# Kernel optimization log

Hardware: AMD Instinct MI355X
Metric: run time of the kernel (lower is better)

Reference implementation:

```python
import jax, jax.numpy as jnp
import numpy as np

N, E, D, H, L, FF = 50000, 500000, 128, 8, 2, 512
HD = D // H  # head dim = 16


def setup_inputs() -> dict:
    key = jax.random.key(0)
    ks = jax.random.split(key, 16)
    inp = {
        "x": jax.random.normal(ks[0], (N, D), jnp.float32),
        "edge_index": jax.random.randint(ks[1], (2, E), 0, N, jnp.int32),
    }
    def w(k, shape, fan_in):
        return jax.random.normal(k, shape, jnp.float32) / np.float32(np.sqrt(fan_in))
    inp["Wq"] = w(ks[2], (L, D, D), D)
    inp["Wk"] = w(ks[3], (L, D, D), D)
    inp["Wv"] = w(ks[4], (L, D, D), D)
    inp["Wo"] = w(ks[5], (L, D, D), D)
    inp["Wpos"] = w(ks[6], (L, D, D), D)
    inp["Wdeg"] = w(ks[7], (L, 1, D), 1)
    inp["W1"] = w(ks[8], (L, D, FF), D)
    inp["W2"] = w(ks[9], (L, FF, D), FF)
    for name, shape in [("bq", (L, D)), ("bk", (L, D)), ("bv", (L, D)),
                        ("bo", (L, D)), ("bpos", (L, D)), ("bdeg", (L, D)),
                        ("ln1_b", (L, D)), ("ln2_b", (L, D)),
                        ("b1", (L, FF)), ("b2", (L, D))]:
        inp[name] = jnp.zeros(shape, jnp.float32)
    inp["ln1_g"] = jnp.ones((L, D), jnp.float32)
    inp["ln2_g"] = jnp.ones((L, D), jnp.float32)
    return inp


def _layernorm(x, g, b):
    mu = jnp.mean(x, axis=-1, keepdims=True)
    var = jnp.mean(jnp.square(x - mu), axis=-1, keepdims=True)
    return (x - mu) * jax.lax.rsqrt(var + 1e-5) * g + b


def _forward(edge_index, x, Wq, bq, Wk, bk, Wv, bv, Wo, bo, Wpos, bpos,
             Wdeg, bdeg, ln1_g, ln1_b, ln2_g, ln2_b, W1, b1, W2, b2):
    n = x.shape[0]
    loops = jnp.arange(n, dtype=edge_index.dtype)
    src = jnp.concatenate([edge_index[0], loops])  # [E+N]
    dst = jnp.concatenate([edge_index[1], loops])  # [E+N]
    scale = np.float32(np.sqrt(HD))
    for l in range(L):
        # pre-attention LayerNorm
        xn = _layernorm(x, ln1_g[l], ln1_b[l])
        # positional encoding: x + proj(x) + deg_proj(standardized degree)
        deg = jax.ops.segment_sum(jnp.ones_like(src, dtype=x.dtype), src, num_segments=n)
        deg = (deg - deg.mean()) / (jnp.std(deg, ddof=1) + 1e-6)
        pos = xn @ Wpos[l] + bpos[l] + deg[:, None] * Wdeg[l][0] + bdeg[l]
        xp = xn + pos
        # per-node QKV projections (linear => identical to per-edge projection)
        q = (xp @ Wq[l] + bq[l]).reshape(n, H, HD)
        k = (xp @ Wk[l] + bk[l]).reshape(n, H, HD)
        v = (xp @ Wv[l] + bv[l]).reshape(n, H, HD)
        # per-edge attention logits  [E+N, H]
        att = jnp.einsum('ehd,ehd->eh', q[dst], k[src]) / scale
        att = jnp.nan_to_num(jnp.clip(att, -50.0, 50.0), nan=0.0, posinf=50.0, neginf=-50.0)
        # segment softmax over destination nodes (every node has a self loop)
        m = jax.ops.segment_max(att, dst, num_segments=n)        # [N, H]
        ex = jnp.exp(att - m[dst])
        s = jax.ops.segment_sum(ex, dst, num_segments=n)
        alpha = ex / (s[dst] + 1e-16)                             # [E+N, H]
        # weighted aggregation + output projection
        msg = (v[src] * alpha[:, :, None]).reshape(-1, D)         # [E+N, D]
        aggr = jax.ops.segment_sum(msg, dst, num_segments=n)      # [N, D]
        x = x + (aggr @ Wo[l] + bo[l])
        # FFN sublayer
        h = jax.nn.gelu(_layernorm(x, ln2_g[l], ln2_b[l]) @ W1[l] + b1[l], approximate=False)
        x = x + (h @ W2[l] + b2[l])
    return x


def reference(x, edge_index, Wq, bq, Wk, bk, Wv, bv, Wo, bo, Wpos, bpos,
              Wdeg, bdeg, ln1_g, ln1_b, ln2_g, ln2_b, W1, b1, W2, b2):
    return _forward(edge_index, x, Wq, bq, Wk, bk, Wv, bv, Wo, bo, Wpos, bpos,
                    Wdeg, bdeg, ln1_g, ln1_b, ln2_g, ln2_b, W1, b1, W2, b2)
```

## Files before the change

### kernel.cpp

```cpp
#include <hip/hip_runtime.h>
#include <hip/hip_bf16.h>
#include <hip/hip_fp16.h>
#include <math.h>

#define DMODEL 128
#define NHEAD 8
#define HEADD 16
#define NLAYER 2
#define FFDIM 512
#define MPAD 50048
#define QKVW 384

using short8 = __attribute__((ext_vector_type(8))) short;
using half8  = __attribute__((ext_vector_type(8))) _Float16;
using f32x4  = __attribute__((ext_vector_type(4))) float;

static __device__ __forceinline__ unsigned short f2h(float f) {
    __half h = __float2half(f);
    unsigned short u; __builtin_memcpy(&u, &h, 2); return u;
}
static __device__ __forceinline__ float h2f(unsigned short u) {
    __half h; __builtin_memcpy(&h, &u, 2); return __half2float(h);
}
static __device__ __forceinline__ half8 s2h8(short8 s) {
    half8 h; __builtin_memcpy(&h, &s, 16); return h;
}
static __device__ __forceinline__ f32x4 MFMAH(short8 a, short8 b, f32x4 c) {
    return __builtin_amdgcn_mfma_f32_16x16x32_f16(s2h8(a), s2h8(b), c, 0, 0, 0);
}
static __device__ __forceinline__ float gelu_fast(float v) {
    float u = v * (0.7978845608f + 0.0356774081f * v * v);
    float t = 1.0f - 2.0f / (1.0f + __expf(2.0f * u));
    return 0.5f * v * (1.0f + t);
}

__global__ __launch_bounds__(256)
void ln_kernel(const float* __restrict__ x, const float* __restrict__ g,
               const float* __restrict__ b, unsigned short* __restrict__ out, int n)
{
    int wave = threadIdx.x >> 6;
    int lane = threadIdx.x & 63;
    int row  = blockIdx.x * 4 + wave;
    if (row >= n) return;
    float2 xv = *(const float2*)(x + (size_t)row * DMODEL + lane * 2);
    float s  = xv.x + xv.y;
    float ss = xv.x * xv.x + xv.y * xv.y;
    #pragma unroll
    for (int d = 1; d < 64; d <<= 1) {
        s  += __shfl_xor(s, d);
        ss += __shfl_xor(ss, d);
    }
    float mu   = s * (1.0f / 128.0f);
    float var  = ss * (1.0f / 128.0f) - mu * mu;
    float rstd = rsqrtf(var + 1e-5f);
    float2 gv = *(const float2*)(g + lane * 2);
    float2 bv = *(const float2*)(b + lane * 2);
    ushort2 o;
    o.x = f2h((xv.x - mu) * rstd * gv.x + bv.x);
    o.y = f2h((xv.y - mu) * rstd * gv.y + bv.y);
    *(ushort2*)(out + (size_t)row * DMODEL + lane * 2) = o;
}

__global__ void wconv_all(const float* __restrict__ Wq, const float* __restrict__ Wk,
                          const float* __restrict__ Wv, const float* __restrict__ Wo,
                          const float* __restrict__ Wpos, const float* __restrict__ W1,
                          const float* __restrict__ W2,
                          unsigned short* __restrict__ wqkvt, unsigned short* __restrict__ wot,
                          unsigned short* __restrict__ wpt, unsigned short* __restrict__ w1t,
                          unsigned short* __restrict__ w2t)
{
    const int DD = NLAYER * DMODEL * DMODEL;
    const int DF = NLAYER * DMODEL * FFDIM;
    int i = blockIdx.x * 256 + threadIdx.x;
    if (i < 3 * DD) {
        int w = i / DD, r = i - w * DD;
        const float* src = (w == 0) ? Wq : (w == 1 ? Wk : Wv);
        int l = r >> 14, rr = r & 16383;
        int k = rr >> 7, nn = rr & 127;
        wqkvt[(size_t)l * QKVW * DMODEL + (size_t)(w * 128 + nn) * DMODEL + k] = f2h(src[r]);
    } else if (i < 5 * DD) {
        int w = (i - 3 * DD) / DD, r = (i - 3 * DD) - w * DD;
        const float* src = (w == 0) ? Wo : Wpos;
        unsigned short* dst = (w == 0) ? wot : wpt;
        int l = r >> 14, rr = r & 16383;
        int k = rr >> 7, nn = rr & 127;
        dst[(size_t)l * DMODEL * DMODEL + (size_t)nn * DMODEL + k] = f2h(src[r]);
    } else if (i < 5 * DD + DF) {
        int r = i - 5 * DD;
        int l = r >> 16, rr = r & 65535;
        int k = rr >> 9, nn = rr & 511;
        w1t[(size_t)l * FFDIM * DMODEL + (size_t)nn * DMODEL + k] = f2h(W1[r]);
    } else if (i < 5 * DD + 2 * DF) {
        int r = i - 5 * DD - DF;
        int l = r >> 16, rr = r & 65535;
        int k = rr >> 7, nn = rr & 127;
        w2t[(size_t)l * DMODEL * FFDIM + (size_t)nn * FFDIM + k] = f2h(W2[r]);
    }
}

__global__ void init_all(float* __restrict__ deg, int* __restrict__ counts,
                         float* __restrict__ stats, int n)
{
    int i = blockIdx.x * 256 + threadIdx.x;
    if (i < n) { deg[i] = 1.0f; counts[i] = 0; }
    if (i == 0) stats[0] = 0.f;
}

__global__ void edge_count(const int* __restrict__ ei, float* __restrict__ deg,
                           int* __restrict__ counts, int e, int n)
{
    int i = blockIdx.x * 256 + threadIdx.x;
    if (i < e) {
        atomicAdd(&deg[ei[i]], 1.0f);
        atomicAdd(&counts[ei[e + i]], 1);
    } else if (i < e + n) {
        atomicAdd(&counts[i - e], 1);
    }
}

__global__ __launch_bounds__(256)
void deg_var(const float* __restrict__ deg, float* __restrict__ stats, float mean, int n)
{
    float acc = 0.f;
    for (int i = blockIdx.x * blockDim.x + threadIdx.x; i < n; i += gridDim.x * blockDim.x) {
        float d = deg[i] - mean;
        acc += d * d;
    }
    #pragma unroll
    for (int d = 1; d < 64; d <<= 1) acc += __shfl_xor(acc, d);
    __shared__ float wsum[4];
    int lane = threadIdx.x & 63, wv = threadIdx.x >> 6;
    if (lane == 0) wsum[wv] = acc;
    __syncthreads();
    if (threadIdx.x == 0) atomicAdd(stats, wsum[0] + wsum[1] + wsum[2] + wsum[3]);
}

__global__ __launch_bounds__(256)
void scan_block(const int* __restrict__ in, int* __restrict__ out,
                int* __restrict__ sums, int n)
{
    __shared__ int buf[2][256];
    int t = threadIdx.x;
    int i = blockIdx.x * 256 + t;
    int v = (i < n) ? in[i] : 0;
    buf[0][t] = v;
    __syncthreads();
    int cur = 0;
    #pragma unroll
    for (int d = 1; d < 256; d <<= 1) {
        int val = buf[cur][t] + ((t >= d) ? buf[cur][t - d] : 0);
        buf[cur ^ 1][t] = val;
        cur ^= 1;
        __syncthreads();
    }
    if (i < n) out[i] = buf[cur][t] - v;
    if (t == 255 && sums) sums[blockIdx.x] = buf[cur][255];
}

__global__ void scan_add(int* __restrict__ offs, int* __restrict__ cursor,
                         const int* __restrict__ carry, int n)
{
    int i = blockIdx.x * 256 + threadIdx.x;
    if (i < n) {
        int v = offs[i] + carry[blockIdx.x];
        offs[i] = v;
        cursor[i] = v;
    }
}

__global__ void csr_fill(const int* __restrict__ ei, int* __restrict__ cursor,
                         int* __restrict__ csr_src, int e, int n)
{
    int i = blockIdx.x * 256 + threadIdx.x;
    if (i >= e + n) return;
    int d, s;
    if (i < e) { s = ei[i]; d = ei[e + i]; }
    else       { s = d = i - e; }
    int pos = atomicAdd(&cursor[d], 1);
    csr_src[pos] = s;
}

static __device__ __forceinline__ void ep_resln(
    f32x4 (&acc)[2][4], float* sm, int row0,
    int wr, int wc, int quad, int l15,
    const float* __restrict__ bias, const float* __restrict__ g,
    const float* __restrict__ bb,
    float* __restrict__ x, unsigned short* __restrict__ lnout, int n)
{
    #pragma unroll
    for (int i = 0; i < 2; ++i) {
        #pragma unroll
        for (int rr = 0; rr < 4; ++rr) {
            int rl = wr * 32 + i * 16 + quad * 4 + rr;
            size_t gr = (size_t)row0 + rl;
            float ps = 0.f, pq = 0.f;
            #pragma unroll
            for (int j = 0; j < 4; ++j) {
                int gc = wc * 64 + j * 16 + l15;
                float xv = (gr < (size_t)n) ? x[gr * DMODEL + gc] : 0.f;
                float v = acc[i][j][rr] + bias[gc] + xv;
                acc[i][j][rr] = v;
                ps += v; pq += v * v;
            }
            ps += __shfl_xor(ps, 1); pq += __shfl_xor(pq, 1);
            ps += __shfl_xor(ps, 2); pq += __shfl_xor(pq, 2);
            ps += __shfl_xor(ps, 4); pq += __shfl_xor(pq, 4);
            ps += __shfl_xor(ps, 8); pq += __shfl_xor(pq, 8);
            if (l15 == 0) { sm[(rl * 2 + wc) * 2 + 0] = ps; sm[(rl * 2 + wc) * 2 + 1] = pq; }
        }
    }
    __syncthreads();
    #pragma unroll
    for (int i = 0; i < 2; ++i) {
        #pragma unroll
        for (int rr = 0; rr < 4; ++rr) {
            int rl = wr * 32 + i * 16 + quad * 4 + rr;
            size_t gr = (size_t)row0 + rl;
            if (gr >= (size_t)n) continue;
            float su = sm[(rl * 2 + 0) * 2 + 0] + sm[(rl * 2 + 1) * 2 + 0];
            float sq = sm[(rl * 2 + 0) * 2 + 1] + sm[(rl * 2 + 1) * 2 + 1];
            float mu   = su * (1.f / 128.f);
            float var  = sq * (1.f / 128.f) - mu * mu;
            float rstd = rsqrtf(var + 1e-5f);
            #pragma unroll
            for (int j = 0; j < 4; ++j) {
                int gc = wc * 64 + j * 16 + l15;
                float v = acc[i][j][rr];
                x[gr * DMODEL + gc] = v;
                lnout[gr * DMODEL + gc] = f2h((v - mu) * rstd * g[gc] + bb[gc]);
            }
        }
    }
}

__global__ __launch_bounds__(256)
void pos_qkv(const unsigned short* __restrict__ xnb,
             const unsigned short* __restrict__ wpos,
             const unsigned short* __restrict__ wqkv,
             const float* __restrict__ bpos,
             const float* __restrict__ deg, const float* __restrict__ stats, float mean,
             const float* __restrict__ wdeg, const float* __restrict__ bdeg,
             const float* __restrict__ bq, const float* __restrict__ bk,
             const float* __restrict__ bv,
             unsigned short* __restrict__ qkv, int n)
{
    __shared__ __align__(16) unsigned short As[64 * 130];
    __shared__ __align__(16) unsigned short Bs[128 * 130];

    const int tid = threadIdx.x, wave = tid >> 6, lane = tid & 63;
    const int wr = wave >> 1, wc = wave & 1, quad = lane >> 4, l15 = lane & 15;
    const int row0 = blockIdx.x * 64;

    #pragma unroll
    for (int c = 0; c < 4; ++c) {
        int g = tid + c * 256; int r = g >> 4, col8 = g & 15;
        *(short8*)&As[r * 130 + col8 * 8] =
            *(const short8*)(xnb + (size_t)(row0 + r) * DMODEL + col8 * 8);
    }
    #pragma unroll
    for (int c = 0; c < 8; ++c) {
        int g = tid + c * 256; int r = g >> 4, col8 = g & 15;
        *(short8*)&Bs[r * 130 + col8 * 8] =
            *(const short8*)(wpos + (size_t)r * DMODEL + col8 * 8);
    }
    __syncthreads();

    short8 af[2][4], bfr[4][4];
    #pragma unroll
    for (int i = 0; i < 2; ++i)
        #pragma unroll
        for (int ks = 0; ks < 4; ++ks)
            af[i][ks] = *(const short8*)&As[(wr * 32 + i * 16 + l15) * 130 + (ks * 4 + quad) * 8];
    #pragma unroll
    for (int j = 0; j < 4; ++j)
        #pragma unroll
        for (int ks = 0; ks < 4; ++ks)
            bfr[j][ks] = *(const short8*)&Bs[(wc * 64 + j * 16 + l15) * 130 + (ks * 4 + quad) * 8];
    __syncthreads();

    f32x4 acc[2][4] = {};
    #pragma unroll
    for (int ks = 0; ks < 4; ++ks)
        #pragma unroll
        for (int i = 0; i < 2; ++i)
            #pragma unroll
            for (int j = 0; j < 4; ++j)
                acc[i][j] = MFMAH(af[i][ks], bfr[j][ks], acc[i][j]);

    {
        float sdv = sqrtf(stats[0] / (float)(n - 1)) + 1e-6f;
        #pragma unroll
        for (int i = 0; i < 2; ++i) {
            #pragma unroll
            for (int rr = 0; rr < 4; ++rr) {
                int rl = wr * 32 + i * 16 + quad * 4 + rr;
                size_t gr = (size_t)row0 + rl;
                if (gr >= (size_t)n) continue;
                float dg = (deg[gr] - mean) / sdv;
                #pragma unroll
                for (int j = 0; j < 4; ++j) {
                    int gc = wc * 64 + j * 16 + l15;
                    float xn = h2f(As[rl * 130 + gc]);
                    float val = acc[i][j][rr] + bpos[gc] + dg * wdeg[gc] + bdeg[gc] + xn;
                    As[rl * 130 + gc] = f2h(val);
                }
            }
        }
    }
    __syncthreads();

    short8 af2[2][4];
    #pragma unroll
    for (int i = 0; i < 2; ++i)
        #pragma unroll
        for (int ks = 0; ks < 4; ++ks)
            af2[i][ks] = *(const short8*)&As[(wr * 32 + i * 16 + l15) * 130 + (ks * 4 + quad) * 8];
    __syncthreads();

    #pragma unroll
    for (int c = 0; c < 3; ++c) {
        #pragma unroll
        for (int cc = 0; cc < 8; ++cc) {
            int g = tid + cc * 256; int r = g >> 4, col8 = g & 15;
            *(short8*)&Bs[r * 130 + col8 * 8] =
                *(const short8*)(wqkv + (size_t)(c * 128 + r) * DMODEL + col8 * 8);
        }
        __syncthreads();
        short8 bf2[4][4];
        #pragma unroll
        for (int j = 0; j < 4; ++j)
            #pragma unroll
            for (int ks = 0; ks < 4; ++ks)
                bf2[j][ks] = *(const short8*)&Bs[(wc * 64 + j * 16 + l15) * 130 + (ks * 4 + quad) * 8];

        f32x4 a2[2][4] = {};
        #pragma unroll
        for (int ks = 0; ks < 4; ++ks)
            #pragma unroll
            for (int i = 0; i < 2; ++i)
                #pragma unroll
                for (int j = 0; j < 4; ++j)
                    a2[i][j] = MFMAH(af2[i][ks], bf2[j][ks], a2[i][j]);

        const float* bp = (c == 0) ? bq : (c == 1 ? bk : bv);
        #pragma unroll
        for (int i = 0; i < 2; ++i) {
            #pragma unroll
            for (int rr = 0; rr < 4; ++rr) {
                size_t gr = (size_t)row0 + wr * 32 + i * 16 + quad * 4 + rr;
                if (gr >= (size_t)n) continue;
                #pragma unroll
                for (int j = 0; j < 4; ++j) {
                    int col = wc * 64 + j * 16 + l15;
                    float val = a2[i][j][rr] + bp[col];
                    int idx = (c == 0) ? col
                            : (128 + ((col >> 1) << 2) + ((c - 1) << 1) + (col & 1));
                    qkv[gr * (size_t)QKVW + idx] = f2h(val);
                }
            }
        }
        if (c < 2) __syncthreads();
    }
}

template<int MODE, int KCH, int TPB>
__global__ __launch_bounds__(256)
void gemm_bres(const unsigned short* __restrict__ A, int strideA,
               const unsigned short* __restrict__ Bt, int strideB,
               const float* __restrict__ bias,
               const float* __restrict__ lng, const float* __restrict__ lnb,
               float* __restrict__ outf, unsigned short* __restrict__ outb,
               int outStride, int n)
{
    __shared__ __align__(16) unsigned short As[64 * 130];
    __shared__ __align__(16) unsigned short Bs[128 * 130];
    __shared__ float sm[64 * 2 * 2];

    const int tid  = threadIdx.x;
    const int wave = tid >> 6, lane = tid & 63;
    const int wr = wave >> 1, wc = wave & 1;
    const int quad = lane >> 4, l15 = lane & 15;
    const int bc = blockIdx.y * 128;

    f32x4 acc[2][4] = {};
    short8 bfr[4][4];
    short8 pr[4];

    {
        const int row0 = blockIdx.x * TPB * 64;
        #pragma unroll
        for (int c = 0; c < 4; ++c) {
            int g = tid + c * 256;
            int r = g >> 4, col8 = g & 15;
            pr[c] = *(const short8*)(A + (size_t)(row0 + r) * strideA + col8 * 8);
        }
    }

    for (int ky = 0; ky < KCH; ++ky) {
        const int kOff = ky * 128;
        #pragma unroll
        for (int c = 0; c < 8; ++c) {
            int g = tid + c * 256;
            int r = g >> 4, col8 = g & 15;
            *(short8*)&Bs[r * 130 + col8 * 8] =
                *(const short8*)(Bt + (size_t)(bc + r) * strideB + kOff + col8 * 8);
        }
        for (int t = 0; t < TPB; ++t) {
            #pragma unroll
            for (int c = 0; c < 4; ++c) {
                int g = tid + c * 256;
                int r = g >> 4, col8 = g & 15;
                *(short8*)&As[r * 130 + col8 * 8] = pr[c];
            }
            {
                int nt = t + 1, nky = ky;
                if (nt == TPB) { nt = 0; nky = ky + 1; }
                if (nky < KCH) {
                    const int nrow0 = (blockIdx.x * TPB + nt) * 64;
                    const int nkOff = nky * 128;
                    #pragma unroll
                    for (int c = 0; c < 4; ++c) {
                        int g = tid + c * 256;
                        int r = g >> 4, col8 = g & 15;
                        pr[c] = *(const short8*)(A + (size_t)(nrow0 + r) * strideA + nkOff + col8 * 8);
                    }
                }
            }
            __syncthreads();
            if (t == 0) {
                #pragma unroll
                for (int j = 0; j < 4; ++j)
                    #pragma unroll
                    for (int ks = 0; ks < 4; ++ks)
                        bfr[j][ks] = *(const short8*)&Bs[(wc * 64 + j * 16 + l15) * 130 + (ks * 4 + quad) * 8];
            }
            if (KCH == 1) {
                #pragma unroll
                for (int i = 0; i < 2; ++i)
                    #pragma unroll
                    for (int j = 0; j < 4; ++j)
                        acc[i][j] = f32x4{0.f, 0.f, 0.f, 0.f};
            }
            short8 af[2][4];
            #pragma unroll
            for (int i = 0; i < 2; ++i)
                #pragma unroll
                for (int ks = 0; ks < 4; ++ks)
                    af[i][ks] = *(const short8*)&As[(wr * 32 + i * 16 + l15) * 130 + (ks * 4 + quad) * 8];
            #pragma unroll
            for (int ks = 0; ks < 4; ++ks)
                #pragma unroll
                for (int i = 0; i < 2; ++i)
                    #pragma unroll
                    for (int j = 0; j < 4; ++j)
                        acc[i][j] = MFMAH(af[i][ks], bfr[j][ks], acc[i][j]);

            if (KCH == 1) {
                const int row0 = (blockIdx.x * TPB + t) * 64;
                if (MODE == 5) {
                    ep_resln(acc, sm, row0, wr, wc, quad, l15, bias, lng, lnb, outf, outb, n);
                } else {
                    #pragma unroll
                    for (int i = 0; i < 2; ++i) {
                        #pragma unroll
                        for (int rr = 0; rr < 4; ++rr) {
                            size_t gr = (size_t)row0 + wr * 32 + i * 16 + quad * 4 + rr;
                            if (gr >= (size_t)n) continue;
                            #pragma unroll
                            for (int j = 0; j < 4; ++j) {
                                int col = wc * 64 + j * 16 + l15;
                                int gc  = bc + col;
                                float val = acc[i][j][rr];
                                if (MODE == 1) {
                                    float* px = outf + gr * (size_t)outStride + gc;
                                    *px = *px + val + bias[gc];
                                } else if (MODE == 2) {
                                    val = gelu_fast(val + bias[gc]);
                                    outb[gr * (size_t)outStride + gc] = f2h(val);
                                }
                            }
                        }
                    }
                }
            }
            __syncthreads();
        }
    }

    if (KCH > 1) {
        const int row0 = blockIdx.x * TPB * 64;
        if (MODE == 5) {
            ep_resln(acc, sm, row0, wr, wc, quad, l15, bias, lng, lnb, outf, outb, n);
        } else {
            #pragma unroll
            for (int i = 0; i < 2; ++i) {
                #pragma unroll
                for (int rr = 0; rr < 4; ++rr) {
                    size_t gr = (size_t)row0 + wr * 32 + i * 16 + quad * 4 + rr;
                    if (gr >= (size_t)n) continue;
                    #pragma unroll
                    for (int j = 0; j < 4; ++j) {
                        int col = wc * 64 + j * 16 + l15;
                        int gc  = bc + col;
                        if (MODE == 1) {
                            float* px = outf + gr * (size_t)outStride + gc;
                            *px = *px + acc[i][j][rr] + bias[gc];
                        }
                    }
                }
            }
        }
    }
}

__global__ __launch_bounds__(256)
void attn_kernel(const unsigned short* __restrict__ qkv,
                 const int* __restrict__ csr_src, const int* __restrict__ offs,
                 const int* __restrict__ counts,
                 unsigned short* __restrict__ aggr, int n)
{
    int wave = threadIdx.x >> 6;
    int lane = threadIdx.x & 63;
    int node = blockIdx.x * 4 + wave;
    if (node >= n) return;

    ushort2 qu = *(const ushort2*)(qkv + (size_t)node * QKVW + lane * 2);
    float qx = h2f(qu.x), qy = h2f(qu.y);
    int beg = offs[node], cnt = counts[node];

    const unsigned short* kvbase = qkv + DMODEL + lane * 4;

    float m = -1e30f, s = 0.f, ax = 0.f, ay = 0.f;
    ushort4 kvA = {0,0,0,0}, kvB = {0,0,0,0};
    int jn0 = 0, jn1 = 0;
    {
        int j0 = csr_src[beg];
        kvA = *(const ushort4*)(kvbase + (size_t)j0 * QKVW);
        if (cnt > 1) {
            int j1 = csr_src[beg + 1];
            kvB = *(const ushort4*)(kvbase + (size_t)j1 * QKVW);
        }
        if (cnt > 3)      { jn0 = csr_src[beg + 2]; jn1 = csr_src[beg + 3]; }
        else if (cnt > 2) { jn0 = csr_src[beg + 2]; }
    }
    int t = 0;
    for (; t + 1 < cnt; t += 2) {
        ushort4 k0 = kvA, k1 = kvB;
        int rem = cnt - t - 2;
        if (rem >= 2) {
            kvA = *(const ushort4*)(kvbase + (size_t)jn0 * QKVW);
            kvB = *(const ushort4*)(kvbase + (size_t)jn1 * QKVW);
        } else if (rem == 1) {
            kvA = *(const ushort4*)(kvbase + (size_t)jn0 * QKVW);
        }
        if (cnt > t + 5)      { jn0 = csr_src[beg + t + 4]; jn1 = csr_src[beg + t + 5]; }
        else if (cnt > t + 4) { jn0 = csr_src[beg + t + 4]; }
        float p0 = qx * h2f(k0.x) + qy * h2f(k0.y);
        float p1 = qx * h2f(k1.x) + qy * h2f(k1.y);
        p0 += __shfl_xor(p0, 1); p1 += __shfl_xor(p1, 1);
        p0 += __shfl_xor(p0, 2); p1 += __shfl_xor(p1, 2);
        p0 += __shfl_xor(p0, 4); p1 += __shfl_xor(p1, 4);
        p0 *= 0.25f; p1 *= 0.25f;
        p0 = (p0 != p0) ? 0.f : fminf(fmaxf(p0, -50.f), 50.f);
        p1 = (p1 != p1) ? 0.f : fminf(fmaxf(p1, -50.f), 50.f);
        float nm = fmaxf(m, fmaxf(p0, p1));
        float sc = __expf(m - nm);
        float e0 = __expf(p0 - nm), e1 = __expf(p1 - nm);
        s  = s  * sc + e0 + e1;
        ax = ax * sc + e0 * h2f(k0.z) + e1 * h2f(k1.z);
        ay = ay * sc + e0 * h2f(k0.w) + e1 * h2f(k1.w);
        m = nm;
    }
    if (t < cnt) {
        float p0 = qx * h2f(kvA.x) + qy * h2f(kvA.y);
        p0 += __shfl_xor(p0, 1); p0 += __shfl_xor(p0, 2); p0 += __shfl_xor(p0, 4);
        p0 *= 0.25f;
        p0 = (p0 != p0) ? 0.f : fminf(fmaxf(p0, -50.f), 50.f);
        float nm = fmaxf(m, p0);
        float sc = __expf(m - nm), e0 = __expf(p0 - nm);
        s = s * sc + e0;
        ax = ax * sc + e0 * h2f(kvA.z);
        ay = ay * sc + e0 * h2f(kvA.w);
        m = nm;
    }
    float r = 1.0f / (s + 1e-16f);
    ushort2 o;
    o.x = f2h(ax * r);
    o.y = f2h(ay * r);
    *(ushort2*)(aggr + (size_t)node * DMODEL + lane * 2) = o;
}

extern "C" void kernel_launch(void* const* d_in, const int* in_sizes, int n_in,
                              void* d_out, int out_size, void* d_ws, size_t ws_size,
                              hipStream_t stream)
{
    const float* x_in  = (const float*)d_in[0];
    const int*   ei    = (const int*)d_in[1];
    const float* Wq    = (const float*)d_in[2];
    const float* Wk    = (const float*)d_in[3];
    const float* Wv    = (const float*)d_in[4];
    const float* Wo    = (const float*)d_in[5];
    const float* Wpos  = (const float*)d_in[6];
    const float* Wdeg  = (const float*)d_in[7];
    const float* W1    = (const float*)d_in[8];
    const float* W2    = (const float*)d_in[9];
    const float* bq    = (const float*)d_in[10];
    const float* bk    = (const float*)d_in[11];
    const float* bv    = (const float*)d_in[12];
    const float* bo    = (const float*)d_in[13];
    const float* bpos  = (const float*)d_in[14];
    const float* bdeg  = (const float*)d_in[15];
    const float* ln1_b = (const float*)d_in[16];
    const float* ln2_b = (const float*)d_in[17];
    const float* b1    = (const float*)d_in[18];
    const float* b2    = (const float*)d_in[19];
    const float* ln1_g = (const float*)d_in[20];
    const float* ln2_g = (const float*)d_in[21];

    const int n   = in_sizes[0] / DMODEL;
    const int e   = in_sizes[1] / 2;
    const int tot = e + n;

    float* x = (float*)d_out;

    char* p = (char*)d_ws;
    auto alloc = [&](size_t bytes) -> void* {
        void* r = (void*)p;
        p += (bytes + 255) & ~(size_t)255;
        return r;
    };
    float* deg     = (float*)alloc((size_t)n * 4);
    float* stats   = (float*)alloc(256);
    int*   counts  = (int*)alloc((size_t)n * 4);
    int*   offs    = (int*)alloc((size_t)n * 4);
    int*   cursor  = (int*)alloc((size_t)n * 4);
    int*   bsums   = (int*)alloc(1024);
    int*   carry   = (int*)alloc(1024);
    int*   csr_src = (int*)alloc((size_t)tot * 4);
    unsigned short* xnb  = (unsigned short*)alloc((size_t)MPAD * DMODEL * 2);
    unsigned short* aggr = (unsigned short*)alloc((size_t)MPAD * DMODEL * 2);
    unsigned short* qkv  = (unsigned short*)alloc((size_t)MPAD * QKVW * 2);
    unsigned short* hb   = (unsigned short*)alloc((size_t)MPAD * FFDIM * 2);
    unsigned short* wqkvt = (unsigned short*)alloc((size_t)NLAYER * QKVW * DMODEL * 2);
    unsigned short* wot  = (unsigned short*)alloc((size_t)NLAYER * DMODEL * DMODEL * 2);
    unsigned short* wpt  = (unsigned short*)alloc((size_t)NLAYER * DMODEL * DMODEL * 2);
    unsigned short* w1t  = (unsigned short*)alloc((size_t)NLAYER * DMODEL * FFDIM * 2);
    unsigned short* w2t  = (unsigned short*)alloc((size_t)NLAYER * FFDIM * DMODEL * 2);

    const int nb_n = (n + 255) / 256;
    const int nb_t = (tot + 255) / 256;
    const int nscan = nb_n;

    hipMemcpyAsync(x, x_in, (size_t)n * DMODEL * 4, hipMemcpyDeviceToDevice, stream);

    {
        const int totalW = 5 * NLAYER * DMODEL * DMODEL + 2 * NLAYER * DMODEL * FFDIM;
        wconv_all<<<(totalW + 255) / 256, 256, 0, stream>>>(Wq, Wk, Wv, Wo, Wpos, W1, W2,
                                                            wqkvt, wot, wpt, w1t, w2t);
    }
    init_all<<<nb_n, 256, 0, stream>>>(deg, counts, stats, n);

    const float mean = (float)((double)tot / (double)n);
    edge_count<<<nb_t, 256, 0, stream>>>(ei, deg, counts, e, n);
    deg_var<<<196, 256, 0, stream>>>(deg, stats, mean, n);

    scan_block<<<nscan, 256, 0, stream>>>(counts, offs, bsums, n);
    scan_block<<<1, 256, 0, stream>>>(bsums, carry, nullptr, nscan);
    scan_add<<<nscan, 256, 0, stream>>>(offs, cursor, carry, n);
    csr_fill<<<nb_t, 256, 0, stream>>>(ei, cursor, csr_src, e, n);

    const int nTiles  = MPAD / 64;
    const int ln_grid = (n + 3) / 4;

    ln_kernel<<<ln_grid, 256, 0, stream>>>(x, ln1_g, ln1_b, xnb, n);

    for (int l = 0; l < NLAYER; ++l) {
        const size_t DD = (size_t)DMODEL * DMODEL;
        const float* wdeg = Wdeg + (size_t)l * DMODEL;
        const unsigned short* wqkv = wqkvt + (size_t)l * QKVW * DMODEL;
        const unsigned short* wo   = wot + l * DD;
        const unsigned short* wpos = wpt + l * DD;
        const unsigned short* w1   = w1t + (size_t)l * DMODEL * FFDIM;
        const unsigned short* w2   = w2t + (size_t)l * FFDIM * DMODEL;

        pos_qkv<<<nTiles, 256, 0, stream>>>(
            xnb, wpos, wqkv,
            bpos + l * DMODEL, deg, stats, mean, wdeg, bdeg + l * DMODEL,
            bq + l * DMODEL, bk + l * DMODEL, bv + l * DMODEL,
            qkv, n);
        attn_kernel<<<ln_grid, 256, 0, stream>>>(qkv, csr_src, offs, counts, aggr, n);
        gemm_bres<5, 1, 1><<<dim3(nTiles, 1), 256, 0, stream>>>(
            aggr, DMODEL, wo, DMODEL,
            bo + l * DMODEL,
            ln2_g + l * DMODEL, ln2_b + l * DMODEL,
            x, xnb, DMODEL, n);
        gemm_bres<2, 1, 1><<<dim3(nTiles, 4), 256, 0, stream>>>(
            xnb, DMODEL, w1, DMODEL,
            b1 + l * FFDIM,
            nullptr, nullptr,
            nullptr, hb, FFDIM, n);
        if (l + 1 < NLAYER) {
            gemm_bres<5, 4, 1><<<dim3(nTiles, 1), 256, 0, stream>>>(
                hb, FFDIM, w2, FFDIM,
                b2 + l * DMODEL,
                ln1_g + (l + 1) * DMODEL, ln1_b + (l + 1) * DMODEL,
                x, xnb, DMODEL, n);
        } else {
            gemm_bres<1, 4, 1><<<dim3(nTiles, 1), 256, 0, stream>>>(
                hb, FFDIM, w2, FFDIM,
                b2 + l * DMODEL,
                nullptr, nullptr,
                x, nullptr, DMODEL, n);
        }
    }
}
```

Before: 546.5 us.

## Replace CSR scan with fixed-stride adjacency and fuse Wo projection with FFN1

The separate scan and fill kernels are removed. The count kernel now writes neighbour ids directly into a fixed 128-slot-per-node adjacency array, saving several launches and passes over the edge list. The Wo projection, residual and LayerNorm are fused with the first FFN GEMM: the normalized tile stays in LDS and never round-trips xnb through global memory. The cost is a larger adjacency buffer with worse locality, and in-degrees above 128 are silently truncated.

```diff
diff --git a/kernel.cpp b/kernel.cpp
--- a/kernel.cpp
+++ b/kernel.cpp
@@ -10,6 +10,7 @@
 #define FFDIM 512
 #define MPAD 50048
 #define QKVW 384
+#define CSTRIDE 128
 
 using short8 = __attribute__((ext_vector_type(8))) short;
 using half8  = __attribute__((ext_vector_type(8))) _Float16;
@@ -98,23 +99,28 @@
     }
 }
 
-__global__ void init_all(float* __restrict__ deg, int* __restrict__ counts,
+__global__ void init_all(float* __restrict__ deg, int* __restrict__ cnt,
                          float* __restrict__ stats, int n)
 {
     int i = blockIdx.x * 256 + threadIdx.x;
-    if (i < n) { deg[i] = 1.0f; counts[i] = 0; }
+    if (i < n) { deg[i] = 1.0f; cnt[i] = 0; }
     if (i == 0) stats[0] = 0.f;
 }
 
-__global__ void edge_count(const int* __restrict__ ei, float* __restrict__ deg,
-                           int* __restrict__ counts, int e, int n)
+__global__ void build_graph(const int* __restrict__ ei, float* __restrict__ deg,
+                            int* __restrict__ cnt, int* __restrict__ csr2,
+                            int e, int n)
 {
     int i = blockIdx.x * 256 + threadIdx.x;
     if (i < e) {
-        atomicAdd(&deg[ei[i]], 1.0f);
-        atomicAdd(&counts[ei[e + i]], 1);
+        int s = ei[i], d = ei[e + i];
+        atomicAdd(&deg[s], 1.0f);
+        int pos = atomicAdd(&cnt[d], 1);
+        if (pos < CSTRIDE) csr2[(size_t)d * CSTRIDE + pos] = s;
     } else if (i < e + n) {
-        atomicAdd(&counts[i - e], 1);
+        int d = i - e;
+        int pos = atomicAdd(&cnt[d], 1);
+        if (pos < CSTRIDE) csr2[(size_t)d * CSTRIDE + pos] = d;
     }
 }
 
@@ -133,51 +139,6 @@
     if (lane == 0) wsum[wv] = acc;
     __syncthreads();
     if (threadIdx.x == 0) atomicAdd(stats, wsum[0] + wsum[1] + wsum[2] + wsum[3]);
-}
-
-__global__ __launch_bounds__(256)
-void scan_block(const int* __restrict__ in, int* __restrict__ out,
-                int* __restrict__ sums, int n)
-{
-    __shared__ int buf[2][256];
-    int t = threadIdx.x;
-    int i = blockIdx.x * 256 + t;
-    int v = (i < n) ? in[i] : 0;
-    buf[0][t] = v;
-    __syncthreads();
-    int cur = 0;
-    #pragma unroll
-    for (int d = 1; d < 256; d <<= 1) {
-        int val = buf[cur][t] + ((t >= d) ? buf[cur][t - d] : 0);
-        buf[cur ^ 1][t] = val;
-        cur ^= 1;
-        __syncthreads();
-    }
-    if (i < n) out[i] = buf[cur][t] - v;
-    if (t == 255 && sums) sums[blockIdx.x] = buf[cur][255];
-}
-
-__global__ void scan_add(int* __restrict__ offs, int* __restrict__ cursor,
-                         const int* __restrict__ carry, int n)
-{
-    int i = blockIdx.x * 256 + threadIdx.x;
-    if (i < n) {
-        int v = offs[i] + carry[blockIdx.x];
-        offs[i] = v;
-        cursor[i] = v;
-    }
-}
-
-__global__ void csr_fill(const int* __restrict__ ei, int* __restrict__ cursor,
-                         int* __restrict__ csr_src, int e, int n)
-{
-    int i = blockIdx.x * 256 + threadIdx.x;
-    if (i >= e + n) return;
-    int d, s;
-    if (i < e) { s = ei[i]; d = ei[e + i]; }
-    else       { s = d = i - e; }
-    int pos = atomicAdd(&cursor[d], 1);
-    csr_src[pos] = s;
 }
 
 static __device__ __forceinline__ void ep_resln(
@@ -228,6 +189,59 @@
                 float v = acc[i][j][rr];
                 x[gr * DMODEL + gc] = v;
                 lnout[gr * DMODEL + gc] = f2h((v - mu) * rstd * g[gc] + bb[gc]);
+            }
+        }
+    }
+}
+
+static __device__ __forceinline__ void ep_resln_lds(
+    f32x4 (&acc)[2][4], float* sm, int row0,
+    int wr, int wc, int quad, int l15,
+    const float* __restrict__ bias, const float* __restrict__ g,
+    const float* __restrict__ bb,
+    float* __restrict__ x, unsigned short* AsLds, int n)
+{
+    #pragma unroll
+    for (int i = 0; i < 2; ++i) {
+        #pragma unroll
+        for (int rr = 0; rr < 4; ++rr) {
+            int rl = wr * 32 + i * 16 + quad * 4 + rr;
+            size_t gr = (size_t)row0 + rl;
+            float ps = 0.f, pq = 0.f;
+            #pragma unroll
+            for (int j = 0; j < 4; ++j) {
+                int gc = wc * 64 + j * 16 + l15;
+                float xv = (gr < (size_t)n) ? x[gr * DMODEL + gc] : 0.f;
+                float v = acc[i][j][rr] + bias[gc] + xv;
+                acc[i][j][rr] = v;
+                ps += v; pq += v * v;
+            }
+            ps += __shfl_xor(ps, 1); pq += __shfl_xor(pq, 1);
+            ps += __shfl_xor(ps, 2); pq += __shfl_xor(pq, 2);
+            ps += __shfl_xor(ps, 4); pq += __shfl_xor(pq, 4);
+            ps += __shfl_xor(ps, 8); pq += __shfl_xor(pq, 8);
+            if (l15 == 0) { sm[(rl * 2 + wc) * 2 + 0] = ps; sm[(rl * 2 + wc) * 2 + 1] = pq; }
+        }
+    }
+    __syncthreads();
+    #pragma unroll
+    for (int i = 0; i < 2; ++i) {
+        #pragma unroll
+        for (int rr = 0; rr < 4; ++rr) {
+            int rl = wr * 32 + i * 16 + quad * 4 + rr;
+            size_t gr = (size_t)row0 + rl;
+            if (gr >= (size_t)n) continue;
+            float su = sm[(rl * 2 + 0) * 2 + 0] + sm[(rl * 2 + 1) * 2 + 0];
+            float sq = sm[(rl * 2 + 0) * 2 + 1] + sm[(rl * 2 + 1) * 2 + 1];
+            float mu   = su * (1.f / 128.f);
+            float var  = sq * (1.f / 128.f) - mu * mu;
+            float rstd = rsqrtf(var + 1e-5f);
+            #pragma unroll
+            for (int j = 0; j < 4; ++j) {
+                int gc = wc * 64 + j * 16 + l15;
+                float v = acc[i][j][rr];
+                x[gr * DMODEL + gc] = v;
+                AsLds[rl * 130 + gc] = f2h((v - mu) * rstd * g[gc] + bb[gc]);
             }
         }
     }
@@ -360,6 +374,109 @@
             }
         }
         if (c < 2) __syncthreads();
+    }
+}
+
+__global__ __launch_bounds__(256)
+void wo_ffn1(const unsigned short* __restrict__ aggr,
+             const unsigned short* __restrict__ wo, const float* __restrict__ bo,
+             const float* __restrict__ lng, const float* __restrict__ lnb,
+             const unsigned short* __restrict__ w1, const float* __restrict__ b1,
+             float* __restrict__ x, unsigned short* __restrict__ hb, int n)
+{
+    __shared__ __align__(16) unsigned short As[64 * 130];
+    __shared__ __align__(16) unsigned short Bs[128 * 130];
+    __shared__ float sm[64 * 2 * 2];
+
+    const int tid = threadIdx.x, wave = tid >> 6, lane = tid & 63;
+    const int wr = wave >> 1, wc = wave & 1, quad = lane >> 4, l15 = lane & 15;
+    const int row0 = blockIdx.x * 64;
+
+    #pragma unroll
+    for (int c = 0; c < 4; ++c) {
+        int g = tid + c * 256; int r = g >> 4, col8 = g & 15;
+        *(short8*)&As[r * 130 + col8 * 8] =
+            *(const short8*)(aggr + (size_t)(row0 + r) * DMODEL + col8 * 8);
+    }
+    #pragma unroll
+    for (int c = 0; c < 8; ++c) {
+        int g = tid + c * 256; int r = g >> 4, col8 = g & 15;
+        *(short8*)&Bs[r * 130 + col8 * 8] =
+            *(const short8*)(wo + (size_t)r * DMODEL + col8 * 8);
+    }
+    __syncthreads();
+
+    short8 af[2][4], bfr[4][4];
+    #pragma unroll
+    for (int i = 0; i < 2; ++i)
+        #pragma unroll
+        for (int ks = 0; ks < 4; ++ks)
+            af[i][ks] = *(const short8*)&As[(wr * 32 + i * 16 + l15) * 130 + (ks * 4 + quad) * 8];
+    #pragma unroll
+    for (int j = 0; j < 4; ++j)
+        #pragma unroll
+        for (int ks = 0; ks < 4; ++ks)
+            bfr[j][ks] = *(const short8*)&Bs[(wc * 64 + j * 16 + l15) * 130 + (ks * 4 + quad) * 8];
+
+    f32x4 acc[2][4] = {};
+    #pragma unroll
+    for (int ks = 0; ks < 4; ++ks)
+        #pragma unroll
+        for (int i = 0; i < 2; ++i)
+            #pragma unroll
+            for (int j = 0; j < 4; ++j)
+                acc[i][j] = MFMAH(af[i][ks], bfr[j][ks], acc[i][j]);
+
+    ep_resln_lds(acc, sm, row0, wr, wc, quad, l15, bo, lng, lnb, x, As, n);
+    __syncthreads();
+
+    short8 af2[2][4];
+    #pragma unroll
+    for (int i = 0; i < 2; ++i)
+        #pragma unroll
+        for (int ks = 0; ks < 4; ++ks)
+            af2[i][ks] = *(const short8*)&As[(wr * 32 + i * 16 + l15) * 130 + (ks * 4 + quad) * 8];
+
+    #pragma unroll
+    for (int c = 0; c < 4; ++c) {
+        #pragma unroll
+        for (int cc = 0; cc < 8; ++cc) {
+            int g = tid + cc * 256; int r = g >> 4, col8 = g & 15;
+            *(short8*)&Bs[r * 130 + col8 * 8] =
+                *(const short8*)(w1 + (size_t)(c * 128 + r) * DMODEL + col8 * 8);
+        }
+        __syncthreads();
+        short8 bf2[4][4];
+        #pragma unroll
+        for (int j = 0; j < 4; ++j)
+            #pragma unroll
+            for (int ks = 0; ks < 4; ++ks)
+                bf2[j][ks] = *(const short8*)&Bs[(wc * 64 + j * 16 + l15) * 130 + (ks * 4 + quad) * 8];
+
+        f32x4 a2[2][4] = {};
+        #pragma unroll
+        for (int ks = 0; ks < 4; ++ks)
+            #pragma unroll
+            for (int i = 0; i < 2; ++i)
+                #pragma unroll
+                for (int j = 0; j < 4; ++j)
+                    a2[i][j] = MFMAH(af2[i][ks], bf2[j][ks], a2[i][j]);
+
+        #pragma unroll
+        for (int i = 0; i < 2; ++i) {
+            #pragma unroll
+            for (int rr = 0; rr < 4; ++rr) {
+                size_t gr = (size_t)row0 + wr * 32 + i * 16 + quad * 4 + rr;
+                if (gr >= (size_t)n) continue;
+                #pragma unroll
+                for (int j = 0; j < 4; ++j) {
+                    int gcol = c * 128 + wc * 64 + j * 16 + l15;
+                    float val = gelu_fast(a2[i][j][rr] + b1[gcol]);
+                    hb[gr * (size_t)FFDIM + gcol] = f2h(val);
+                }
+            }
+        }
+        if (c < 3) __syncthreads();
     }
 }
 
@@ -434,13 +551,6 @@
                     for (int ks = 0; ks < 4; ++ks)
                         bfr[j][ks] = *(const short8*)&Bs[(wc * 64 + j * 16 + l15) * 130 + (ks * 4 + quad) * 8];
             }
-            if (KCH == 1) {
-                #pragma unroll
-                for (int i = 0; i < 2; ++i)
-                    #pragma unroll
-                    for (int j = 0; j < 4; ++j)
-                        acc[i][j] = f32x4{0.f, 0.f, 0.f, 0.f};
-            }
             short8 af[2][4];
             #pragma unroll
             for (int i = 0; i < 2; ++i)
@@ -454,40 +564,11 @@
                     #pragma unroll
                     for (int j = 0; j < 4; ++j)
                         acc[i][j] = MFMAH(af[i][ks], bfr[j][ks], acc[i][j]);
-
-            if (KCH == 1) {
-                const int row0 = (blockIdx.x * TPB + t) * 64;
-                if (MODE == 5) {
-                    ep_resln(acc, sm, row0, wr, wc, quad, l15, bias, lng, lnb, outf, outb, n);
-                } else {
-                    #pragma unroll
-                    for (int i = 0; i < 2; ++i) {
-                        #pragma unroll
-                        for (int rr = 0; rr < 4; ++rr) {
-                            size_t gr = (size_t)row0 + wr * 32 + i * 16 + quad * 4 + rr;
-                            if (gr >= (size_t)n) continue;
-                            #pragma unroll
-                            for (int j = 0; j < 4; ++j) {
-                                int col = wc * 64 + j * 16 + l15;
-                                int gc  = bc + col;
-                                float val = acc[i][j][rr];
-                                if (MODE == 1) {
-                                    float* px = outf + gr * (size_t)outStride + gc;
-                                    *px = *px + val + bias[gc];
-                                } else if (MODE == 2) {
-                                    val = gelu_fast(val + bias[gc]);
-                                    outb[gr * (size_t)outStride + gc] = f2h(val);
-                                }
-                            }
-                        }
-                    }
-                }
-            }
             __syncthreads();
         }
     }
 
-    if (KCH > 1) {
+    {
         const int row0 = blockIdx.x * TPB * 64;
         if (MODE == 5) {
             ep_resln(acc, sm, row0, wr, wc, quad, l15, bias, lng, lnb, outf, outb, n);
@@ -502,10 +583,8 @@
                     for (int j = 0; j < 4; ++j) {
                         int col = wc * 64 + j * 16 + l15;
                         int gc  = bc + col;
-                        if (MODE == 1) {
-                            float* px = outf + gr * (size_t)outStride + gc;
-                            *px = *px + acc[i][j][rr] + bias[gc];
-                        }
+                        float* px = outf + gr * (size_t)outStride + gc;
+                        *px = *px + acc[i][j][rr] + bias[gc];
                     }
                 }
             }
@@ -515,8 +594,7 @@
 
 __global__ __launch_bounds__(256)
 void attn_kernel(const unsigned short* __restrict__ qkv,
-                 const int* __restrict__ csr_src, const int* __restrict__ offs,
-                 const int* __restrict__ counts,
+                 const int* __restrict__ csr2, const int* __restrict__ cntarr,
                  unsigned short* __restrict__ aggr, int n)
 {
     int wave = threadIdx.x >> 6;
@@ -526,7 +604,9 @@
 
     ushort2 qu = *(const ushort2*)(qkv + (size_t)node * QKVW + lane * 2);
     float qx = h2f(qu.x), qy = h2f(qu.y);
-    int beg = offs[node], cnt = counts[node];
+    const int* src = csr2 + (size_t)node * CSTRIDE;
+    int cnt = cntarr[node];
+    if (cnt > CSTRIDE) cnt = CSTRIDE;
 
     const unsigned short* kvbase = qkv + DMODEL + lane * 4;
 
@@ -534,14 +614,14 @@
     ushort4 kvA = {0,0,0,0}, kvB = {0,0,0,0};
     int jn0 = 0, jn1 = 0;
     {
-        int j0 = csr_src[beg];
+        int j0 = src[0];
         kvA = *(const ushort4*)(kvbase + (size_t)j0 * QKVW);
         if (cnt > 1) {
-            int j1 = csr_src[beg + 1];
+            int j1 = src[1];
             kvB = *(const ushort4*)(kvbase + (size_t)j1 * QKVW);
         }
-        if (cnt > 3)      { jn0 = csr_src[beg + 2]; jn1 = csr_src[beg + 3]; }
-        else if (cnt > 2) { jn0 = csr_src[beg + 2]; }
+        if (cnt > 3)      { jn0 = src[2]; jn1 = src[3]; }
+        else if (cnt > 2) { jn0 = src[2]; }
     }
     int t = 0;
     for (; t + 1 < cnt; t += 2) {
@@ -553,8 +633,8 @@
         } else if (rem == 1) {
             kvA = *(const ushort4*)(kvbase + (size_t)jn0 * QKVW);
         }
-        if (cnt > t + 5)      { jn0 = csr_src[beg + t + 4]; jn1 = csr_src[beg + t + 5]; }
-        else if (cnt > t + 4) { jn0 = csr_src[beg + t + 4]; }
+        if (cnt > t + 5)      { jn0 = src[t + 4]; jn1 = src[t + 5]; }
+        else if (cnt > t + 4) { jn0 = src[t + 4]; }
         float p0 = qx * h2f(k0.x) + qy * h2f(k0.y);
         float p1 = qx * h2f(k1.x) + qy * h2f(k1.y);
         p0 += __shfl_xor(p0, 1); p1 += __shfl_xor(p1, 1);
@@ -631,12 +711,8 @@
     };
     float* deg     = (float*)alloc((size_t)n * 4);
     float* stats   = (float*)alloc(256);
-    int*   counts  = (int*)alloc((size_t)n * 4);
-    int*   offs    = (int*)alloc((size_t)n * 4);
-    int*   cursor  = (int*)alloc((size_t)n * 4);
-    int*   bsums   = (int*)alloc(1024);
-    int*   carry   = (int*)alloc(1024);
-    int*   csr_src = (int*)alloc((size_t)tot * 4);
+    int*   cnt     = (int*)alloc((size_t)n * 4);
+    int*   csr2    = (int*)alloc((size_t)MPAD * CSTRIDE * 4);
     unsigned short* xnb  = (unsigned short*)alloc((size_t)MPAD * DMODEL * 2);
     unsigned short* aggr = (unsigned short*)alloc((size_t)MPAD * DMODEL * 2);
     unsigned short* qkv  = (unsigned short*)alloc((size_t)MPAD * QKVW * 2);
@@ -649,7 +725,6 @@
 
     const int nb_n = (n + 255) / 256;
     const int nb_t = (tot + 255) / 256;
-    const int nscan = nb_n;
 
     hipMemcpyAsync(x, x_in, (size_t)n * DMODEL * 4, hipMemcpyDeviceToDevice, stream);
 
@@ -658,16 +733,11 @@
         wconv_all<<<(totalW + 255) / 256, 256, 0, stream>>>(Wq, Wk, Wv, Wo, Wpos, W1, W2,
                                                             wqkvt, wot, wpt, w1t, w2t);
     }
-    init_all<<<nb_n, 256, 0, stream>>>(deg, counts, stats, n);
+    init_all<<<nb_n, 256, 0, stream>>>(deg, cnt, stats, n);
 
     const float mean = (float)((double)tot / (double)n);
-    edge_count<<<nb_t, 256, 0, stream>>>(ei, deg, counts, e, n);
+    build_graph<<<nb_t, 256, 0, stream>>>(ei, deg, cnt, csr2, e, n);
     deg_var<<<196, 256, 0, stream>>>(deg, stats, mean, n);
-
-    scan_block<<<nscan, 256, 0, stream>>>(counts, offs, bsums, n);
-    scan_block<<<1, 256, 0, stream>>>(bsums, carry, nullptr, nscan);
-    scan_add<<<nscan, 256, 0, stream>>>(offs, cursor, carry, n);
-    csr_fill<<<nb_t, 256, 0, stream>>>(ei, cursor, csr_src, e, n);
 
     const int nTiles  = MPAD / 64;
     const int ln_grid = (n + 3) / 4;
@@ -688,17 +758,12 @@
             bpos + l * DMODEL, deg, stats, mean, wdeg, bdeg + l * DMODEL,
             bq + l * DMODEL, bk + l * DMODEL, bv + l * DMODEL,
             qkv, n);
-        attn_kernel<<<ln_grid, 256, 0, stream>>>(qkv, csr_src, offs, counts, aggr, n);
-        gemm_bres<5, 1, 1><<<dim3(nTiles, 1), 256, 0, stream>>>(
-            aggr, DMODEL, wo, DMODEL,
-            bo + l * DMODEL,
+        attn_kernel<<<ln_grid, 256, 0, stream>>>(qkv, csr2, cnt, aggr, n);
+        wo_ffn1<<<nTiles, 256, 0, stream>>>(
+            aggr, wo, bo + l * DMODEL,
             ln2_g + l * DMODEL, ln2_b + l * DMODEL,
-            x, xnb, DMODEL, n);
-        gemm_bres<2, 1, 1><<<dim3(nTiles, 4), 256, 0, stream>>>(
-            xnb, DMODEL, w1, DMODEL,
-            b1 + l * FFDIM,
-            nullptr, nullptr,
-            nullptr, hb, FFDIM, n);
+            w1, b1 + l * FFDIM,
+            x, hb, n);
         if (l + 1 < NLAYER) {
             gemm_bres<5, 4, 1><<<dim3(nTiles, 1), 256, 0, stream>>>(
                 hb, FFDIM, w2, FFDIM,
```

After: 525.3 us. 1.04x faster.
